# Kernel optimization log

Hardware: AMD Instinct MI355X
Metric: run time of the kernel (lower is better)

## Reference

```python
import jax, jax.numpy as jnp
import numpy as np

D_MODEL = 1024
D_COND = 512
N_HEADS = 16
D_HEAD = D_MODEL // N_HEADS
DIM_FF = 4 * D_MODEL
EPS = 1e-5


def setup_inputs() -> dict:
    key = jax.random.key(0)
    ks = jax.random.split(key, 12)
    B, S = 2, 2048
    s = 0.02
    return {
        "x": jax.random.normal(ks[0], (B, S, D_MODEL), jnp.float32),
        "cond": jax.random.normal(ks[1], (B, S, D_COND), jnp.float32),
        # AdaLN1 proj (stored as (in, out) so y = h @ W + b)
        "p1_w": jax.random.normal(ks[2], (D_COND, 2 * D_MODEL), jnp.float32) * s,
        "p1_b": jax.random.normal(ks[3], (2 * D_MODEL,), jnp.float32) * s,
        "qkv_w": jax.random.normal(ks[4], (D_MODEL, 3 * D_MODEL), jnp.float32) * s,
        "attn_out_w": jax.random.normal(ks[5], (D_MODEL, D_MODEL), jnp.float32) * s,
        "p2_w": jax.random.normal(ks[6], (D_COND, 2 * D_MODEL), jnp.float32) * s,
        "p2_b": jax.random.normal(ks[7], (2 * D_MODEL,), jnp.float32) * s,
        "ffn_w1": jax.random.normal(ks[8], (D_MODEL, DIM_FF), jnp.float32) * s,
        "ffn_b1": jax.random.normal(ks[9], (DIM_FF,), jnp.float32) * s,
        "ffn_w2": jax.random.normal(ks[10], (DIM_FF, D_MODEL), jnp.float32) * s,
        "ffn_b2": jax.random.normal(ks[11], (D_MODEL,), jnp.float32) * s,
    }


def _adaln(x, cond, w, b):
    # LayerNorm without affine, then (1+gamma)*xn + beta with gamma,beta from cond
    gb = jax.nn.silu(cond) @ w + b            # (B,S,2D)
    gamma, beta = jnp.split(gb, 2, axis=-1)
    mu = jnp.mean(x, axis=-1, keepdims=True)
    var = jnp.mean((x - mu) ** 2, axis=-1, keepdims=True)
    xn = (x - mu) * jax.lax.rsqrt(var + EPS)
    return xn * (1.0 + gamma) + beta


def reference(x, cond, p1_w, p1_b, qkv_w, attn_out_w, p2_w, p2_b,
              ffn_w1, ffn_b1, ffn_w2, ffn_b2):
    B, S, D = x.shape
    H, d = N_HEADS, D_HEAD
    scale = d ** -0.5

    residual = x
    h = _adaln(x, cond, p1_w, p1_b)
    qkv = h @ qkv_w                            # (B,S,3D)
    q, k, v = jnp.split(qkv, 3, axis=-1)
    q = q.reshape(B, S, H, d).transpose(0, 2, 1, 3)   # (B,H,S,d)
    k = k.reshape(B, S, H, d).transpose(0, 2, 1, 3)
    v = v.reshape(B, S, H, d).transpose(0, 2, 1, 3)

    scores = jnp.einsum("bhqd,bhkd->bhqk", q, k) * scale
    attn = jax.nn.softmax(scores, axis=-1)
    out = jnp.einsum("bhqk,bhkd->bhqd", attn, v)      # (B,H,S,d)
    out = out.transpose(0, 2, 1, 3).reshape(B, S, D)
    x = residual + out @ attn_out_w

    residual = x
    h = _adaln(x, cond, p2_w, p2_b)
    ff = jax.nn.gelu(h @ ffn_w1 + ffn_b1, approximate=False) @ ffn_w2 + ffn_b2
    return residual + ff
```

## Files before the change

### kernel.cpp

```cpp
#include <hip/hip_runtime.h>
#include <math.h>

#define D_MODEL 1024
#define SEQ 2048
#define NTOK 4096

typedef __attribute__((ext_vector_type(8))) short bf16x8;
typedef __attribute__((ext_vector_type(4))) float f32x4;

__device__ __forceinline__ unsigned short f2bf(float f) {
    union { float f; unsigned u; } v; v.f = f;
    unsigned r = v.u + 0x7FFFu + ((v.u >> 16) & 1u);
    return (unsigned short)(r >> 16);
}
__device__ __forceinline__ float bf2f(unsigned short u) {
    union { unsigned u; float f; } v; v.u = ((unsigned)u) << 16; return v.f;
}
__device__ __forceinline__ unsigned cvt_pk_bf16(float x, float y) {
    unsigned r;
    asm("v_cvt_pk_bf16_f32 %0, %1, %2" : "=v"(r) : "v"(x), "v"(y));
    return r;
}

__device__ __forceinline__ void ld_g2l(const void* g, void* l) {
    __builtin_amdgcn_global_load_lds(
        (const __attribute__((address_space(1))) void*)g,
        (__attribute__((address_space(3))) void*)l, 16, 0, 0);
}

__global__ __launch_bounds__(256) void prep_weights(
    const float* __restrict__ p1, const float* __restrict__ p2,
    const float* __restrict__ qkvw, const float* __restrict__ attnw,
    const float* __restrict__ f1, const float* __restrict__ f2,
    const float* __restrict__ cond,
    unsigned short* __restrict__ wt_cond, unsigned short* __restrict__ wt_qkv,
    unsigned short* __restrict__ wt_attn, unsigned short* __restrict__ wt_ffn1,
    unsigned short* __restrict__ wt_ffn2, unsigned short* __restrict__ siluc)
{
    const int t = blockIdx.x;
    if (t >= 3584) {
        const int base = (t - 3584) * 1024 + threadIdx.x;
#pragma unroll
        for (int i = 0; i < 4; i++) {
            const int idx = base + i * 256;
            float4 v = ((const float4*)cond)[idx];
            ushort4 o;
            o.x = f2bf(v.x / (1.f + expf(-v.x)));
            o.y = f2bf(v.y / (1.f + expf(-v.y)));
            o.z = f2bf(v.z / (1.f + expf(-v.z)));
            o.w = f2bf(v.w / (1.f + expf(-v.w)));
            ((ushort4*)siluc)[idx] = o;
        }
        return;
    }
    const float* src; unsigned short* dst; int K, N, lt;
    if (t < 512)       { src = (t < 256) ? p1 : p2;
                         dst = wt_cond + (t < 256 ? 0 : 2048 * 512);
                         K = 512;  N = 2048; lt = t & 255; }
    else if (t < 1280) { src = qkvw;  dst = wt_qkv;  K = 1024; N = 3072; lt = t - 512; }
    else if (t < 1536) { src = attnw; dst = wt_attn; K = 1024; N = 1024; lt = t - 1280; }
    else if (t < 2560) { src = f1;    dst = wt_ffn1; K = 1024; N = 4096; lt = t - 1536; }
    else               { src = f2;    dst = wt_ffn2; K = 4096; N = 1024; lt = t - 2560; }
    const int ntile = N >> 6;
    const int n0 = (lt % ntile) * 64, k0 = (lt / ntile) * 64;

    __shared__ float tile[64][65];
    const int tx = threadIdx.x & 15, ty = threadIdx.x >> 4;
#pragma unroll
    for (int i = 0; i < 4; i++) {
        const int k = ty + i * 16;
        float4 v = *(const float4*)&src[(size_t)(k0 + k) * N + n0 + tx * 4];
        tile[k][tx * 4 + 0] = v.x; tile[k][tx * 4 + 1] = v.y;
        tile[k][tx * 4 + 2] = v.z; tile[k][tx * 4 + 3] = v.w;
    }
    __syncthreads();
#pragma unroll
    for (int i = 0; i < 4; i++) {
        const int n = ty + i * 16;
        ushort4 o;
        o.x = f2bf(tile[tx * 4 + 0][n]); o.y = f2bf(tile[tx * 4 + 1][n]);
        o.z = f2bf(tile[tx * 4 + 2][n]); o.w = f2bf(tile[tx * 4 + 3][n]);
        *(ushort4*)&dst[(size_t)(n0 + n) * K + k0 + tx * 4] = o;
    }
}

#define EPI_GB   0
#define EPI_QKV  1
#define EPI_PROJ 2
#define EPI_FFN1 3
#define EPI_FFN2 4

template<int EPI, int BM>
__global__ __launch_bounds__(256, 4) void gemm_bf16(
    const unsigned short* __restrict__ A,
    const unsigned short* __restrict__ Bt,
    const float* __restrict__ bias, const float* __restrict__ bias2,
    const float* __restrict__ res,
    void* __restrict__ Cv,
    unsigned short* __restrict__ qb, unsigned short* __restrict__ kb,
    unsigned short* __restrict__ vtb,
    int K)
{
    constexpr int WM = BM / 2;
    constexpr int MT = WM / 16;
    __shared__ __align__(16) unsigned short As[BM * 64];
    __shared__ __align__(16) unsigned short Bs[128 * 64];
    const int tid = threadIdx.x;
    const int lane = tid & 63, w = tid >> 6;
    const int cc = lane & 15, quad = lane >> 4;
    const int wm = (w >> 1) * WM, wn = (w & 1) * 64;
    const int m0 = blockIdx.y * BM, n0 = blockIdx.x * 128;

    f32x4 acc[MT][4];
#pragma unroll
    for (int i = 0; i < MT; i++)
#pragma unroll
        for (int j = 0; j < 4; j++) acc[i][j] = (f32x4)0.f;

    for (int k0 = 0; k0 < K; k0 += 64) {
        __syncthreads();
#pragma unroll
        for (int i = 0; i < BM / 32; i++) {
            const int idx = i * 256 + tid;
            const int row = idx >> 3, c = idx & 7;
            const int kc = (c ^ (row & 7)) << 3;
            ld_g2l(&A[(size_t)(m0 + row) * K + k0 + kc], &As[idx << 3]);
        }
#pragma unroll
        for (int i = 0; i < 4; i++) {
            const int idx = i * 256 + tid;
            const int row = idx >> 3, c = idx & 7;
            const int kc = (c ^ (row & 7)) << 3;
            ld_g2l(&Bt[(size_t)(n0 + row) * K + k0 + kc], &Bs[idx << 3]);
        }
        __syncthreads();
#pragma unroll
        for (int ks = 0; ks < 2; ks++) {
            bf16x8 af[MT], bfr[4];
            const int pc = (((ks << 2) | quad) ^ (cc & 7)) << 3;
#pragma unroll
            for (int t = 0; t < MT; t++)
                af[t]  = *(const bf16x8*)&As[(wm + t * 16 + cc) * 64 + pc];
#pragma unroll
            for (int t = 0; t < 4; t++)
                bfr[t] = *(const bf16x8*)&Bs[(wn + t * 16 + cc) * 64 + pc];
#pragma unroll
            for (int mt = 0; mt < MT; mt++)
#pragma unroll
                for (int nt = 0; nt < 4; nt++)
                    acc[mt][nt] = __builtin_amdgcn_mfma_f32_16x16x32_bf16(
                        af[mt], bfr[nt], acc[mt][nt], 0, 0, 0);
        }
    }

    if (EPI == EPI_GB) {
        unsigned short* C = (unsigned short*)Cv;
#pragma unroll
        for (int mt = 0; mt < MT; mt++)
#pragma unroll
        for (int r = 0; r < 4; r++) {
            const int m = m0 + wm + mt * 16 + quad * 4 + r;
#pragma unroll
            for (int nt = 0; nt < 4; nt++) {
                const int n = n0 + wn + nt * 16 + cc;
                const float b = (n < 2048) ? bias[n] : bias2[n - 2048];
                C[(size_t)m * 4096 + n] = f2bf(acc[mt][nt][r] + b);
            }
        }
    } else if (EPI == EPI_PROJ) {
        float* C = (float*)Cv;
#pragma unroll
        for (int mt = 0; mt < MT; mt++)
#pragma unroll
        for (int r = 0; r < 4; r++) {
            const int m = m0 + wm + mt * 16 + quad * 4 + r;
#pragma unroll
            for (int nt = 0; nt < 4; nt++) {
                const int n = n0 + wn + nt * 16 + cc;
                C[(size_t)m * 1024 + n] = acc[mt][nt][r] + res[(size_t)m * 1024 + n];
            }
        }
    } else if (EPI == EPI_FFN1) {
        unsigned short* C = (unsigned short*)Cv;
#pragma unroll
        for (int mt = 0; mt < MT; mt++)
#pragma unroll
        for (int r = 0; r < 4; r++) {
            const int m = m0 + wm + mt * 16 + quad * 4 + r;
#pragma unroll
            for (int nt = 0; nt < 4; nt++) {
                const int n = n0 + wn + nt * 16 + cc;
                float v = acc[mt][nt][r] + bias[n];
                const float u = v + 0.044715f * v * v * v;
                const float g = v / (1.f + exp2f(-2.3022084f * u));
                C[(size_t)m * 4096 + n] = f2bf(g);
            }
        }
    } else if (EPI == EPI_FFN2) {
        float* C = (float*)Cv;
#pragma unroll
        for (int mt = 0; mt < MT; mt++)
#pragma unroll
        for (int r = 0; r < 4; r++) {
            const int m = m0 + wm + mt * 16 + quad * 4 + r;
#pragma unroll
            for (int nt = 0; nt < 4; nt++) {
                const int n = n0 + wn + nt * 16 + cc;
                C[(size_t)m * 1024 + n] = acc[mt][nt][r] + bias[n] + res[(size_t)m * 1024 + n];
            }
        }
    } else {
        const int region = n0 >> 10;
        const int b = m0 >> 11;
        if (region < 2) {
            unsigned short* dst = region ? kb : qb;
            const float sc = region ? 1.0f : 0.125f * 1.44269504088896340736f;
#pragma unroll
            for (int mt = 0; mt < MT; mt++)
#pragma unroll
            for (int r = 0; r < 4; r++) {
                const int m = m0 + wm + mt * 16 + quad * 4 + r;
                const int s = m & 2047;
#pragma unroll
                for (int nt = 0; nt < 4; nt++) {
                    const int n = (n0 + wn + nt * 16 + cc) & 1023;
                    const int hh = n >> 6, d = n & 63;
                    dst[(((size_t)b * 16 + hh) * 2048 + s) * 64 + d] =
                        f2bf(acc[mt][nt][r] * sc);
                }
            }
        } else {
            const int sb = (m0 + wm) & 2047;
#pragma unroll
            for (int mt = 0; mt < MT; mt++) {
                const int kpos = sb + ((mt >> 1) << 5) + (quad << 3) + ((mt & 1) << 2);
#pragma unroll
                for (int nt = 0; nt < 4; nt++) {
                    const int n = (n0 + wn + nt * 16 + cc) & 1023;
                    const int hh = n >> 6, d = n & 63;
                    ushort4 o;
                    o.x = f2bf(acc[mt][nt][0]); o.y = f2bf(acc[mt][nt][1]);
                    o.z = f2bf(acc[mt][nt][2]); o.w = f2bf(acc[mt][nt][3]);
                    *(ushort4*)&vtb[(((size_t)b * 16 + hh) * 64 + d) * 2048 + kpos] = o;
                }
            }
        }
    }
}

__global__ __launch_bounds__(512) void attn_mfma(
    const unsigned short* __restrict__ qb, const unsigned short* __restrict__ kb,
    const unsigned short* __restrict__ vtb,
    unsigned short* __restrict__ Op0, unsigned short* __restrict__ Op1,
    unsigned short* __restrict__ Op2, unsigned short* __restrict__ Op3,
    float* __restrict__ lp)
{
    __shared__ __align__(16) unsigned short ks[64 * 64];
    __shared__ __align__(16) unsigned short vts[64 * 64];

    const int tid = threadIdx.x;
    const int lane = tid & 63, w = tid >> 6;
    const int c = lane & 15, quad = lane >> 4;
    const int bh = blockIdx.y;
    const int q0 = blockIdx.x * 256;
    const int z = blockIdx.z;
    const int kk0 = z * 512;

    bf16x8 qf[2][2];
#pragma unroll
    for (int qs = 0; qs < 2; qs++) {
        const size_t base = (((size_t)bh * 2048) + q0 + w * 32 + qs * 16 + c) * 64 + quad * 8;
        qf[qs][0] = *(const bf16x8*)&qb[base];
        qf[qs][1] = *(const bf16x8*)&qb[base + 32];
    }

    bf16x8 ones;
#pragma unroll
    for (int i = 0; i < 8; i++) ones[i] = (short)0x3F80;

    f32x4 of[2][4];
#pragma unroll
    for (int qs = 0; qs < 2; qs++)
#pragma unroll
        for (int i = 0; i < 4; i++) of[qs][i] = (f32x4)0.f;
    f32x4 lf[2];
    lf[0] = (f32x4)0.f; lf[1] = (f32x4)0.f;

    const size_t kbase = ((size_t)bh * 2048) * 64;
    const size_t vbase = ((size_t)bh * 64) * 2048;

    const int srow = tid >> 3, spc = tid & 7;
    const int slc = spc ^ (srow & 7);

    for (int kk = kk0; kk < kk0 + 512; kk += 64) {
        __syncthreads();
        ld_g2l(&kb[kbase + (size_t)(kk + srow) * 64 + slc * 8], &ks[tid << 3]);
        ld_g2l(&vtb[vbase + (size_t)srow * 2048 + kk + slc * 8], &vts[tid << 3]);
        __syncthreads();

        f32x4 sc[2][4];
#pragma unroll
        for (int qs = 0; qs < 2; qs++)
#pragma unroll
            for (int t = 0; t < 4; t++) sc[qs][t] = (f32x4)0.f;
#pragma unroll
        for (int t = 0; t < 4; t++) {
#pragma unroll
            for (int kh = 0; kh < 2; kh++) {
                const int phys = ((kh * 4 + quad) ^ (c & 7)) << 3;
                bf16x8 kf = *(const bf16x8*)&ks[(t * 16 + c) * 64 + phys];
#pragma unroll
                for (int qs = 0; qs < 2; qs++)
                    sc[qs][t] = __builtin_amdgcn_mfma_f32_16x16x32_bf16(
                        kf, qf[qs][kh], sc[qs][t], 0, 0, 0);
            }
        }

        bf16x8 pb[2][2];
#pragma unroll
        for (int qs = 0; qs < 2; qs++) {
#pragma unroll
            for (int t = 0; t < 4; t++)
#pragma unroll
                for (int r = 0; r < 4; r++)
                    sc[qs][t][r] = exp2f(sc[qs][t][r]);
#pragma unroll
            for (int kh = 0; kh < 2; kh++) {
                union { int4 i; bf16x8 v; } u;
                u.i.x = cvt_pk_bf16(sc[qs][2 * kh][0],     sc[qs][2 * kh][1]);
                u.i.y = cvt_pk_bf16(sc[qs][2 * kh][2],     sc[qs][2 * kh][3]);
                u.i.z = cvt_pk_bf16(sc[qs][2 * kh + 1][0], sc[qs][2 * kh + 1][1]);
                u.i.w = cvt_pk_bf16(sc[qs][2 * kh + 1][2], sc[qs][2 * kh + 1][3]);
                pb[qs][kh] = u.v;
            }
        }

#pragma unroll
        for (int qs = 0; qs < 2; qs++)
#pragma unroll
            for (int kh = 0; kh < 2; kh++)
                lf[qs] = __builtin_amdgcn_mfma_f32_16x16x32_bf16(
                    ones, pb[qs][kh], lf[qs], 0, 0, 0);

#pragma unroll
        for (int dt = 0; dt < 4; dt++) {
#pragma unroll
            for (int kh = 0; kh < 2; kh++) {
                const int phys = ((kh * 4 + quad) ^ (c & 7)) << 3;
                bf16x8 vf = *(const bf16x8*)&vts[(dt * 16 + c) * 64 + phys];
#pragma unroll
                for (int qs = 0; qs < 2; qs++)
                    of[qs][dt] = __builtin_amdgcn_mfma_f32_16x16x32_bf16(
                        vf, pb[qs][kh], of[qs][dt], 0, 0, 0);
            }
        }
    }

    unsigned short* Op = (z == 0) ? Op0 : (z == 1) ? Op1 : (z == 2) ? Op2 : Op3;
    const int b = bh >> 4, hh = bh & 15;
#pragma unroll
    for (int qs = 0; qs < 2; qs++) {
        const int q = q0 + w * 32 + qs * 16 + c;
        if (lane < 16)
            lp[((size_t)z * 32 + bh) * 2048 + q] = lf[qs][0];
        const size_t row = (size_t)(b * 2048 + q);
#pragma unroll
        for (int dt = 0; dt < 4; dt++) {
            ushort4 o;
            o.x = f2bf(of[qs][dt][0]); o.y = f2bf(of[qs][dt][1]);
            o.z = f2bf(of[qs][dt][2]); o.w = f2bf(of[qs][dt][3]);
            *(ushort4*)&Op[row * 1024 + hh * 64 + dt * 16 + quad * 4] = o;
        }
    }
}

__global__ __launch_bounds__(256) void merge_attn(
    const unsigned short* __restrict__ Op0, const unsigned short* __restrict__ Op1,
    const unsigned short* __restrict__ Op2, const unsigned short* __restrict__ Op3,
    const float* __restrict__ lp, unsigned short* __restrict__ attnb)
{
    const int row = blockIdx.x;
    const int b = row >> 11, s = row & 2047;
    const int tid = threadIdx.x;
    const int n = tid * 4, h = tid >> 4;
    float lsum = 0.f;
#pragma unroll
    for (int z = 0; z < 4; z++)
        lsum += lp[((size_t)z * 32 + b * 16 + h) * 2048 + s];
    const float inv = 1.f / lsum;
    const size_t off = (size_t)row * 1024 + n;
    ushort4 a0 = *(const ushort4*)&Op0[off];
    ushort4 a1 = *(const ushort4*)&Op1[off];
    ushort4 a2 = *(const ushort4*)&Op2[off];
    ushort4 a3 = *(const ushort4*)&Op3[off];
    ushort4 o;
    o.x = f2bf((bf2f(a0.x) + bf2f(a1.x) + bf2f(a2.x) + bf2f(a3.x)) * inv);
    o.y = f2bf((bf2f(a0.y) + bf2f(a1.y) + bf2f(a2.y) + bf2f(a3.y)) * inv);
    o.z = f2bf((bf2f(a0.z) + bf2f(a1.z) + bf2f(a2.z) + bf2f(a3.z)) * inv);
    o.w = f2bf((bf2f(a0.w) + bf2f(a1.w) + bf2f(a2.w) + bf2f(a3.w)) * inv);
    *(ushort4*)&attnb[off] = o;
}

__global__ __launch_bounds__(256) void adaln_bf(
    const float* __restrict__ x, const unsigned short* __restrict__ gb, int gboff,
    unsigned short* __restrict__ h)
{
    const int row = blockIdx.x;
    const float* xr = x + (size_t)row * D_MODEL;
    float4 v = ((const float4*)xr)[threadIdx.x];
    float s = v.x + v.y + v.z + v.w;
    float ss = v.x * v.x + v.y * v.y + v.z * v.z + v.w * v.w;
#pragma unroll
    for (int off = 1; off < 64; off <<= 1) {
        s  += __shfl_xor(s, off, 64);
        ss += __shfl_xor(ss, off, 64);
    }
    __shared__ float red[8];
    const int wave = threadIdx.x >> 6;
    if ((threadIdx.x & 63) == 0) { red[wave] = s; red[4 + wave] = ss; }
    __syncthreads();
    s  = red[0] + red[1] + red[2] + red[3];
    ss = red[4] + red[5] + red[6] + red[7];
    const float mu = s * (1.f / 1024.f);
    const float var = ss * (1.f / 1024.f) - mu * mu;
    const float rstd = rsqrtf(var + 1e-5f);
    const int c = threadIdx.x * 4;
    ushort4 g4 = *(const ushort4*)&gb[(size_t)row * 4096 + gboff + c];
    ushort4 b4 = *(const ushort4*)&gb[(size_t)row * 4096 + gboff + 1024 + c];
    ushort4 o;
    o.x = f2bf((v.x - mu) * rstd * (1.f + bf2f(g4.x)) + bf2f(b4.x));
    o.y = f2bf((v.y - mu) * rstd * (1.f + bf2f(g4.y)) + bf2f(b4.y));
    o.z = f2bf((v.z - mu) * rstd * (1.f + bf2f(g4.z)) + bf2f(b4.z));
    o.w = f2bf((v.w - mu) * rstd * (1.f + bf2f(g4.w)) + bf2f(b4.w));
    *(ushort4*)&h[(size_t)row * 1024 + c] = o;
}

extern "C" void kernel_launch(void* const* d_in, const int* in_sizes, int n_in,
                              void* d_out, int out_size, void* d_ws, size_t ws_size,
                              hipStream_t stream)
{
    const float* x      = (const float*)d_in[0];
    const float* cond   = (const float*)d_in[1];
    const float* p1_w   = (const float*)d_in[2];
    const float* p1_b   = (const float*)d_in[3];
    const float* qkv_w  = (const float*)d_in[4];
    const float* attn_w = (const float*)d_in[5];
    const float* p2_w   = (const float*)d_in[6];
    const float* p2_b   = (const float*)d_in[7];
    const float* ffn_w1 = (const float*)d_in[8];
    const float* ffn_b1 = (const float*)d_in[9];
    const float* ffn_w2 = (const float*)d_in[10];
    const float* ffn_b2 = (const float*)d_in[11];
    float* out = (float*)d_out;

    char* ws = (char*)d_ws;
    const size_t MB = 1024ull * 1024ull;
    unsigned short* wt_cond = (unsigned short*)(ws);
    unsigned short* wt_qkv  = (unsigned short*)(ws + 4 * MB);
    unsigned short* wt_attn = (unsigned short*)(ws + 10 * MB);
    unsigned short* wt_ffn1 = (unsigned short*)(ws + 12 * MB);
    unsigned short* wt_ffn2 = (unsigned short*)(ws + 20 * MB);
    unsigned short* siluc   = (unsigned short*)(ws + 28 * MB);
    unsigned short* gb      = (unsigned short*)(ws + 32 * MB);
    unsigned short* h       = (unsigned short*)(ws + 64 * MB);
    float*          x1      = (float*)(ws + 72 * MB);
    unsigned short* qb      = (unsigned short*)(ws + 88 * MB);
    unsigned short* kb      = (unsigned short*)(ws + 96 * MB);
    unsigned short* vtb     = (unsigned short*)(ws + 104 * MB);
    unsigned short* attnb   = (unsigned short*)(ws + 112 * MB);
    unsigned short* ff1     = (unsigned short*)(ws + 88 * MB);
    unsigned short* Op0     = (unsigned short*)(ws);
    unsigned short* Op1     = (unsigned short*)(ws + 64 * MB);
    unsigned short* Op2     = (unsigned short*)(ws + 72 * MB);
    unsigned short* Op3     = (unsigned short*)(ws + 80 * MB);
    float*          lp      = (float*)(ws + 28 * MB);

    dim3 blk(256);

    prep_weights<<<dim3(4096), blk, 0, stream>>>(
        p1_w, p2_w, qkv_w, attn_w, ffn_w1, ffn_w2, cond,
        wt_cond, wt_qkv, wt_attn, wt_ffn1, wt_ffn2, siluc);

    gemm_bf16<EPI_GB, 128><<<dim3(32, 32), blk, 0, stream>>>(
        siluc, wt_cond, p1_b, p2_b, nullptr, gb, nullptr, nullptr, nullptr, 512);
    adaln_bf<<<NTOK, blk, 0, stream>>>(x, gb, 0, h);
    gemm_bf16<EPI_QKV, 128><<<dim3(24, 32), blk, 0, stream>>>(
        h, wt_qkv, nullptr, nullptr, nullptr, nullptr, qb, kb, vtb, 1024);
    attn_mfma<<<dim3(SEQ / 256, 32, 4), dim3(512), 0, stream>>>(
        qb, kb, vtb, Op0, Op1, Op2, Op3, lp);
    merge_attn<<<dim3(NTOK), blk, 0, stream>>>(Op0, Op1, Op2, Op3, lp, attnb);
    gemm_bf16<EPI_PROJ, 64><<<dim3(8, 64), blk, 0, stream>>>(
        attnb, wt_attn, nullptr, nullptr, x, x1, nullptr, nullptr, nullptr, 1024);
    adaln_bf<<<NTOK, blk, 0, stream>>>(x1, gb, 2048, h);
    gemm_bf16<EPI_FFN1, 128><<<dim3(32, 32), blk, 0, stream>>>(
        h, wt_ffn1, ffn_b1, nullptr, nullptr, ff1, nullptr, nullptr, nullptr, 1024);
    gemm_bf16<EPI_FFN2, 64><<<dim3(8, 64), blk, 0, stream>>>(
        ff1, wt_ffn2, ffn_b2, nullptr, x1, out, nullptr, nullptr, nullptr, 4096);
}
```

Baseline: 389.1 us.

## Split-K the FFN2 GEMM into four slices with a separate merge kernel

The FFN2 GEMM (K=4096) is split along K into four slices via a new grid z-dimension, which raises the block count from 512 to 2048 to better fill the GPU. Each slice writes bf16 partial sums into a workspace region freed after the AdaLN stages. A new merge kernel then sums the four partials and adds the bias and residual. This trades roughly 32MB of extra partial-sum write and read traffic, plus an extra launch, for better occupancy. Rounding the partials to bf16 also adds some precision loss.

```diff
diff --git a/kernel.cpp b/kernel.cpp
--- a/kernel.cpp
+++ b/kernel.cpp
@@ -89,8 +89,9 @@
 #define EPI_PROJ 2
 #define EPI_FFN1 3
 #define EPI_FFN2 4
-
-template<int EPI, int BM>
+#define EPI_PART 5
+
+template<int EPI, int BM, int SPLIT = 1>
 __global__ __launch_bounds__(256, 4) void gemm_bf16(
     const unsigned short* __restrict__ A,
     const unsigned short* __restrict__ Bt,
@@ -110,6 +111,8 @@
     const int cc = lane & 15, quad = lane >> 4;
     const int wm = (w >> 1) * WM, wn = (w & 1) * 64;
     const int m0 = blockIdx.y * BM, n0 = blockIdx.x * 128;
+    const int kslice = K / SPLIT;
+    const int kbeg = (SPLIT > 1) ? (int)blockIdx.z * kslice : 0;
 
     f32x4 acc[MT][4];
 #pragma unroll
@@ -117,7 +120,7 @@
 #pragma unroll
         for (int j = 0; j < 4; j++) acc[i][j] = (f32x4)0.f;
 
-    for (int k0 = 0; k0 < K; k0 += 64) {
+    for (int k0 = kbeg; k0 < kbeg + kslice; k0 += 64) {
         __syncthreads();
 #pragma unroll
         for (int i = 0; i < BM / 32; i++) {
@@ -194,6 +197,19 @@
                 const float u = v + 0.044715f * v * v * v;
                 const float g = v / (1.f + exp2f(-2.3022084f * u));
                 C[(size_t)m * 4096 + n] = f2bf(g);
+            }
+        }
+    } else if (EPI == EPI_PART) {
+        unsigned short* C = (unsigned short*)Cv + (size_t)blockIdx.z * (4096ull * 1024ull);
+#pragma unroll
+        for (int mt = 0; mt < MT; mt++)
+#pragma unroll
+        for (int r = 0; r < 4; r++) {
+            const int m = m0 + wm + mt * 16 + quad * 4 + r;
+#pragma unroll
+            for (int nt = 0; nt < 4; nt++) {
+                const int n = n0 + wn + nt * 16 + cc;
+                C[(size_t)m * 1024 + n] = f2bf(acc[mt][nt][r]);
             }
         }
     } else if (EPI == EPI_FFN2) {
@@ -246,6 +262,28 @@
             }
         }
     }
+}
+
+__global__ __launch_bounds__(256) void merge_ffn2(
+    const unsigned short* __restrict__ P, const float* __restrict__ x1,
+    const float* __restrict__ b2, float* __restrict__ out)
+{
+    const size_t idx = (size_t)blockIdx.x * 1024 + (size_t)threadIdx.x * 4;
+    const int n = (int)(idx & 1023);
+    float4 xv = *(const float4*)&x1[idx];
+    float4 bv = *(const float4*)&b2[n];
+    float s0 = 0.f, s1 = 0.f, s2 = 0.f, s3 = 0.f;
+#pragma unroll
+    for (int z = 0; z < 4; z++) {
+        ushort4 p = *(const ushort4*)&P[z * (4096ull * 1024ull) + idx];
+        s0 += bf2f(p.x); s1 += bf2f(p.y); s2 += bf2f(p.z); s3 += bf2f(p.w);
+    }
+    float4 o;
+    o.x = xv.x + bv.x + s0;
+    o.y = xv.y + bv.y + s1;
+    o.z = xv.z + bv.z + s2;
+    o.w = xv.w + bv.w + s3;
+    *(float4*)&out[idx] = o;
 }
 
 __global__ __launch_bounds__(512) void attn_mfma(
@@ -474,6 +512,7 @@
     unsigned short* Op2     = (unsigned short*)(ws + 72 * MB);
     unsigned short* Op3     = (unsigned short*)(ws + 80 * MB);
     float*          lp      = (float*)(ws + 28 * MB);
+    unsigned short* Pff     = (unsigned short*)(ws + 32 * MB);
 
     dim3 blk(256);
 
@@ -494,6 +533,7 @@
     adaln_bf<<<NTOK, blk, 0, stream>>>(x1, gb, 2048, h);
     gemm_bf16<EPI_FFN1, 128><<<dim3(32, 32), blk, 0, stream>>>(
         h, wt_ffn1, ffn_b1, nullptr, nullptr, ff1, nullptr, nullptr, nullptr, 1024);
-    gemm_bf16<EPI_FFN2, 64><<<dim3(8, 64), blk, 0, stream>>>(
-        ff1, wt_ffn2, ffn_b2, nullptr, x1, out, nullptr, nullptr, nullptr, 4096);
-}
+    gemm_bf16<EPI_PART, 64, 4><<<dim3(8, 64, 4), blk, 0, stream>>>(
+        ff1, wt_ffn2, nullptr, nullptr, nullptr, Pff, nullptr, nullptr, nullptr, 4096);
+    merge_ffn2<<<dim3(4096), blk, 0, stream>>>(Pff, x1, ffn_b2, out);
+}
```

Result: slower. 399.4 us (+2.6%).

## Double-buffer LDS tiles in attention and narrow GEMMs to overlap loads

Applied to the files above, without the earlier changes.

Adds a templated double-buffered LDS path to the bf16 GEMM, enabled for the projection and FFN2 GEMMs. It also double-buffers the K/V tiles in the attention kernel, so the next tile is staged while the current one is computed. This drops one barrier per k-step and hides global-to-LDS latency, at the cost of twice the shared memory per block. The attention kernel also gains a minimum-occupancy launch bound, which may cap registers and cause spills. Its score accumulation now starts from a zero constant instead of separately zeroed registers.

```diff
diff --git a/kernel.cpp b/kernel.cpp
--- a/kernel.cpp
+++ b/kernel.cpp
@@ -90,7 +90,7 @@
 #define EPI_FFN1 3
 #define EPI_FFN2 4
 
-template<int EPI, int BM>
+template<int EPI, int BM, bool DBUF = false>
 __global__ __launch_bounds__(256, 4) void gemm_bf16(
     const unsigned short* __restrict__ A,
     const unsigned short* __restrict__ Bt,
@@ -103,8 +103,9 @@
 {
     constexpr int WM = BM / 2;
     constexpr int MT = WM / 16;
-    __shared__ __align__(16) unsigned short As[BM * 64];
-    __shared__ __align__(16) unsigned short Bs[128 * 64];
+    constexpr int NB = DBUF ? 2 : 1;
+    __shared__ __align__(16) unsigned short As[NB][BM * 64];
+    __shared__ __align__(16) unsigned short Bs[NB][128 * 64];
     const int tid = threadIdx.x;
     const int lane = tid & 63, w = tid >> 6;
     const int cc = lane & 15, quad = lane >> 4;
@@ -117,39 +118,57 @@
 #pragma unroll
         for (int j = 0; j < 4; j++) acc[i][j] = (f32x4)0.f;
 
-    for (int k0 = 0; k0 < K; k0 += 64) {
-        __syncthreads();
+    auto stage = [&](int buf, int k0) {
 #pragma unroll
         for (int i = 0; i < BM / 32; i++) {
             const int idx = i * 256 + tid;
             const int row = idx >> 3, c = idx & 7;
             const int kc = (c ^ (row & 7)) << 3;
-            ld_g2l(&A[(size_t)(m0 + row) * K + k0 + kc], &As[idx << 3]);
+            ld_g2l(&A[(size_t)(m0 + row) * K + k0 + kc], &As[buf][idx << 3]);
         }
 #pragma unroll
         for (int i = 0; i < 4; i++) {
             const int idx = i * 256 + tid;
             const int row = idx >> 3, c = idx & 7;
             const int kc = (c ^ (row & 7)) << 3;
-            ld_g2l(&Bt[(size_t)(n0 + row) * K + k0 + kc], &Bs[idx << 3]);
-        }
-        __syncthreads();
+            ld_g2l(&Bt[(size_t)(n0 + row) * K + k0 + kc], &Bs[buf][idx << 3]);
+        }
+    };
+    auto compute = [&](int buf) {
 #pragma unroll
         for (int ks = 0; ks < 2; ks++) {
             bf16x8 af[MT], bfr[4];
             const int pc = (((ks << 2) | quad) ^ (cc & 7)) << 3;
 #pragma unroll
             for (int t = 0; t < MT; t++)
-                af[t]  = *(const bf16x8*)&As[(wm + t * 16 + cc) * 64 + pc];
+                af[t]  = *(const bf16x8*)&As[buf][(wm + t * 16 + cc) * 64 + pc];
 #pragma unroll
             for (int t = 0; t < 4; t++)
-                bfr[t] = *(const bf16x8*)&Bs[(wn + t * 16 + cc) * 64 + pc];
+                bfr[t] = *(const bf16x8*)&Bs[buf][(wn + t * 16 + cc) * 64 + pc];
 #pragma unroll
             for (int mt = 0; mt < MT; mt++)
 #pragma unroll
                 for (int nt = 0; nt < 4; nt++)
                     acc[mt][nt] = __builtin_amdgcn_mfma_f32_16x16x32_bf16(
                         af[mt], bfr[nt], acc[mt][nt], 0, 0, 0);
+        }
+    };
+
+    if (DBUF) {
+        stage(0, 0);
+        int cur = 0;
+        for (int k0 = 0; k0 < K; k0 += 64) {
+            __syncthreads();
+            if (k0 + 64 < K) stage(cur ^ 1, k0 + 64);
+            compute(cur);
+            cur ^= 1;
+        }
+    } else {
+        for (int k0 = 0; k0 < K; k0 += 64) {
+            __syncthreads();
+            stage(0, k0);
+            __syncthreads();
+            compute(0);
         }
     }
 
@@ -248,15 +267,15 @@
     }
 }
 
-__global__ __launch_bounds__(512) void attn_mfma(
+__global__ __launch_bounds__(512, 4) void attn_mfma(
     const unsigned short* __restrict__ qb, const unsigned short* __restrict__ kb,
     const unsigned short* __restrict__ vtb,
     unsigned short* __restrict__ Op0, unsigned short* __restrict__ Op1,
     unsigned short* __restrict__ Op2, unsigned short* __restrict__ Op3,
     float* __restrict__ lp)
 {
-    __shared__ __align__(16) unsigned short ks[64 * 64];
-    __shared__ __align__(16) unsigned short vts[64 * 64];
+    __shared__ __align__(16) unsigned short ks[2][64 * 64];
+    __shared__ __align__(16) unsigned short vts[2][64 * 64];
 
     const int tid = threadIdx.x;
     const int lane = tid & 63, w = tid >> 6;
@@ -277,6 +296,7 @@
     bf16x8 ones;
 #pragma unroll
     for (int i = 0; i < 8; i++) ones[i] = (short)0x3F80;
+    const f32x4 fz = (f32x4)0.f;
 
     f32x4 of[2][4];
 #pragma unroll
@@ -292,28 +312,28 @@
     const int srow = tid >> 3, spc = tid & 7;
     const int slc = spc ^ (srow & 7);
 
+    auto stage = [&](int buf, int kk) {
+        ld_g2l(&kb[kbase + (size_t)(kk + srow) * 64 + slc * 8], &ks[buf][tid << 3]);
+        ld_g2l(&vtb[vbase + (size_t)srow * 2048 + kk + slc * 8], &vts[buf][tid << 3]);
+    };
+
+    stage(0, kk0);
+    int cur = 0;
     for (int kk = kk0; kk < kk0 + 512; kk += 64) {
         __syncthreads();
-        ld_g2l(&kb[kbase + (size_t)(kk + srow) * 64 + slc * 8], &ks[tid << 3]);
-        ld_g2l(&vtb[vbase + (size_t)srow * 2048 + kk + slc * 8], &vts[tid << 3]);
-        __syncthreads();
+        if (kk + 64 < kk0 + 512) stage(cur ^ 1, kk + 64);
 
         f32x4 sc[2][4];
 #pragma unroll
-        for (int qs = 0; qs < 2; qs++)
-#pragma unroll
-            for (int t = 0; t < 4; t++) sc[qs][t] = (f32x4)0.f;
-#pragma unroll
         for (int t = 0; t < 4; t++) {
-#pragma unroll
-            for (int kh = 0; kh < 2; kh++) {
-                const int phys = ((kh * 4 + quad) ^ (c & 7)) << 3;
-                bf16x8 kf = *(const bf16x8*)&ks[(t * 16 + c) * 64 + phys];
-#pragma unroll
-                for (int qs = 0; qs < 2; qs++)
-                    sc[qs][t] = __builtin_amdgcn_mfma_f32_16x16x32_bf16(
-                        kf, qf[qs][kh], sc[qs][t], 0, 0, 0);
-            }
+            const int phys0 = ((0 * 4 + quad) ^ (c & 7)) << 3;
+            const int phys1 = ((1 * 4 + quad) ^ (c & 7)) << 3;
+            bf16x8 kf0 = *(const bf16x8*)&ks[cur][(t * 16 + c) * 64 + phys0];
+            sc[0][t] = __builtin_amdgcn_mfma_f32_16x16x32_bf16(kf0, qf[0][0], fz, 0, 0, 0);
+            sc[1][t] = __builtin_amdgcn_mfma_f32_16x16x32_bf16(kf0, qf[1][0], fz, 0, 0, 0);
+            bf16x8 kf1 = *(const bf16x8*)&ks[cur][(t * 16 + c) * 64 + phys1];
+            sc[0][t] = __builtin_amdgcn_mfma_f32_16x16x32_bf16(kf1, qf[0][1], sc[0][t], 0, 0, 0);
+            sc[1][t] = __builtin_amdgcn_mfma_f32_16x16x32_bf16(kf1, qf[1][1], sc[1][t], 0, 0, 0);
         }
 
         bf16x8 pb[2][2];
@@ -347,13 +367,14 @@
 #pragma unroll
             for (int kh = 0; kh < 2; kh++) {
                 const int phys = ((kh * 4 + quad) ^ (c & 7)) << 3;
-                bf16x8 vf = *(const bf16x8*)&vts[(dt * 16 + c) * 64 + phys];
+                bf16x8 vf = *(const bf16x8*)&vts[cur][(dt * 16 + c) * 64 + phys];
 #pragma unroll
                 for (int qs = 0; qs < 2; qs++)
                     of[qs][dt] = __builtin_amdgcn_mfma_f32_16x16x32_bf16(
                         vf, pb[qs][kh], of[qs][dt], 0, 0, 0);
             }
         }
+        cur ^= 1;
     }
 
     unsigned short* Op = (z == 0) ? Op0 : (z == 1) ? Op1 : (z == 2) ? Op2 : Op3;
@@ -489,11 +510,11 @@
     attn_mfma<<<dim3(SEQ / 256, 32, 4), dim3(512), 0, stream>>>(
         qb, kb, vtb, Op0, Op1, Op2, Op3, lp);
     merge_attn<<<dim3(NTOK), blk, 0, stream>>>(Op0, Op1, Op2, Op3, lp, attnb);
-    gemm_bf16<EPI_PROJ, 64><<<dim3(8, 64), blk, 0, stream>>>(
+    gemm_bf16<EPI_PROJ, 64, true><<<dim3(8, 64), blk, 0, stream>>>(
         attnb, wt_attn, nullptr, nullptr, x, x1, nullptr, nullptr, nullptr, 1024);
     adaln_bf<<<NTOK, blk, 0, stream>>>(x1, gb, 2048, h);
     gemm_bf16<EPI_FFN1, 128><<<dim3(32, 32), blk, 0, stream>>>(
         h, wt_ffn1, ffn_b1, nullptr, nullptr, ff1, nullptr, nullptr, nullptr, 1024);
-    gemm_bf16<EPI_FFN2, 64><<<dim3(8, 64), blk, 0, stream>>>(
+    gemm_bf16<EPI_FFN2, 64, true><<<dim3(8, 64), blk, 0, stream>>>(
         ff1, wt_ffn2, ffn_b2, nullptr, x1, out, nullptr, nullptr, nullptr, 4096);
 }
```

Result: no change. 385.7 us (-0.9%).
